# Kernel optimization log

Hardware: AMD Instinct MI355X
Metric: run time of the kernel (lower is better)

Reference implementation:

```python
import jax, jax.numpy as jnp
import numpy as np

N = 100000      # nodes
E = 1600000     # edges
F_IN = 64       # num_features
H = 64          # nhid
G = 512         # num graphs in batch
C = 2           # num_classes
BN_EPS = 1e-5


def setup_inputs() -> dict:
    key = jax.random.key(0)
    ks = jax.random.split(key, 8)
    x = jax.random.normal(ks[0], (N, F_IN), jnp.float32)
    edge_index = jax.random.randint(ks[1], (2, E), 0, N, dtype=jnp.int64)
    batch = jnp.sort(jax.random.randint(ks[2], (N,), 0, G, dtype=jnp.int64))
    s = lambda k, shp, fan: (jax.random.normal(k, shp, jnp.float32) / np.sqrt(fan)).astype(jnp.float32)
    W1 = s(ks[3], (F_IN, H), F_IN); b1 = jnp.zeros((H,), jnp.float32)
    W2 = s(ks[4], (H, H), H);       b2 = jnp.zeros((H,), jnp.float32)
    Wg = s(ks[5], (H, 1), H);       bg = jnp.zeros((1,), jnp.float32)
    bn_gamma = jnp.ones((H,), jnp.float32); bn_beta = jnp.zeros((H,), jnp.float32)
    bn_mean = jnp.zeros((H,), jnp.float32); bn_var = jnp.ones((H,), jnp.float32)
    W_lin = s(ks[6], (H, C), H);    b_lin = jnp.zeros((C,), jnp.float32)
    return dict(x=x, edge_index=edge_index, batch=batch,
                W1=W1, b1=b1, W2=W2, b2=b2, Wg=Wg, bg=bg,
                bn_gamma=bn_gamma, bn_beta=bn_beta, bn_mean=bn_mean, bn_var=bn_var,
                W_lin=W_lin, b_lin=b_lin)


def reference(x, edge_index, batch, W1, b1, W2, b2, Wg, bg,
              bn_gamma, bn_beta, bn_mean, bn_var, W_lin, b_lin):
    src, dst = edge_index[0], edge_index[1]
    # GINConv (eps=0): h_i = MLP(x_i + sum_{j->i} x_j)
    agg = jax.ops.segment_sum(x[src], dst, num_segments=N)       # [N, F_IN]
    h = x + agg
    h = jnp.maximum(h @ W1 + b1, 0.0) @ W2 + b2                  # [N, H]
    h = jnp.maximum(h, 0.0)                                      # outer ReLU
    # Attentional aggregation: segment softmax of gate, weighted segment-sum
    gate = (h @ Wg + bg)[:, 0]                                   # [N]
    gmax = jax.ops.segment_max(gate, batch, num_segments=G)      # [G]
    ex = jnp.exp(gate - gmax[batch])                             # [N]
    denom = jax.ops.segment_sum(ex, batch, num_segments=G)       # [G]
    alpha = ex / denom[batch]                                    # [N]
    pooled = jax.ops.segment_sum(alpha[:, None] * h, batch, num_segments=G)  # [G, H]
    # BatchNorm1d in eval mode (running stats); dropout is identity in eval
    norm = (pooled - bn_mean) / jnp.sqrt(bn_var + BN_EPS) * bn_gamma + bn_beta
    logits = norm @ W_lin + b_lin                                # [G, C]
    return jax.nn.log_softmax(logits, axis=-1)
```

## Files before the change

### kernel.cpp

```cpp
#include <hip/hip_runtime.h>
#include <math.h>
#include <float.h>

#define BN_EPS 1e-5f
#define PBLK   8192
#define NBUCKP 832
#define ACAP   4096
#define STCAP  3072

typedef short s16x8 __attribute__((ext_vector_type(8)));
typedef float f32x4 __attribute__((ext_vector_type(4)));

__device__ __forceinline__ unsigned short f2bf(float f) {
    unsigned u = __float_as_uint(f);
    u += 0x7FFFu + ((u >> 16) & 1u);
    return (unsigned short)(u >> 16);
}
__device__ __forceinline__ float bf2f(unsigned short b) {
    return __uint_as_float(((unsigned)b) << 16);
}

__global__ __launch_bounds__(256) void prep_partition(
    const float* __restrict__ x, unsigned short* __restrict__ xb,
    const float* __restrict__ W1, const float* __restrict__ W2,
    unsigned short* __restrict__ w1t, unsigned short* __restrict__ w2t,
    const int* __restrict__ src, const int* __restrict__ dst,
    int* __restrict__ bcur0, int* __restrict__ packed2,
    int N, int E)
{
    __shared__ int hist[NBUCKP], lstart[NBUCKP], goff[NBUCKP], cur[NBUCKP];
    __shared__ int sorted[PBLK];
    __shared__ unsigned short sbkt[PBLK];

    int tid = threadIdx.x;
    int lane = tid & 63;
    int blk = blockIdx.x;

    int n4 = N * 16;
    for (int i = blk * 256 + tid; i < n4; i += gridDim.x * 256) {
        float4 f = *(const float4*)(x + (size_t)i * 4);
        ushort4 o;
        o.x = f2bf(f.x); o.y = f2bf(f.y); o.z = f2bf(f.z); o.w = f2bf(f.w);
        *(ushort4*)(xb + (size_t)i * 4) = o;
    }
    if (blk == 0)
        for (int idx = tid; idx < 4096; idx += 256)
            w1t[idx] = f2bf(W1[(idx & 63) * 64 + (idx >> 6)]);
    if (blk == 1)
        for (int idx = tid; idx < 4096; idx += 256)
            w2t[idx] = f2bf(W2[(idx & 63) * 64 + (idx >> 6)]);

    int e0 = blk * PBLK;
    int cnt = E - e0; if (cnt > PBLK) cnt = PBLK; if (cnt < 0) cnt = 0;

    for (int i = tid; i < NBUCKP; i += 256) hist[i] = 0;
    __syncthreads();
    for (int i = tid; i < cnt; i += 256)
        atomicAdd(&hist[dst[e0 + i] >> 7], 1);
    __syncthreads();
    if (tid < 64) {
        int carry = 0;
        #pragma unroll
        for (int c = 0; c < NBUCKP / 64; ++c) {
            int idx = c * 64 + lane;
            int v = hist[idx];
            int xv = v;
            #pragma unroll
            for (int d = 1; d < 64; d <<= 1) {
                int t = __shfl_up(xv, d); if (lane >= d) xv += t;
            }
            lstart[idx] = xv - v + carry;
            carry += __shfl(xv, 63);
        }
    }
    __syncthreads();
    for (int i = tid; i < NBUCKP; i += 256) {
        cur[i] = lstart[i];
        if (hist[i] > 0) goff[i] = atomicAdd(&bcur0[i], hist[i]);
    }
    __syncthreads();
    for (int i = tid; i < cnt; i += 256) {
        int d = dst[e0 + i];
        int s = src[e0 + i];
        int b = d >> 7;
        int p = atomicAdd(&cur[b], 1);
        sorted[p] = ((d & 127) << 17) | s;
        sbkt[p] = (unsigned short)b;
    }
    __syncthreads();
    for (int i = tid; i < cnt; i += 256) {
        int b = sbkt[i];
        packed2[(size_t)b * ACAP + goff[b] + (i - lstart[b])] = sorted[i];
    }
}

__global__ __launch_bounds__(512) void bucket_fused(
    const unsigned short* __restrict__ xb,
    const int* __restrict__ packed2, const int* __restrict__ bcur0,
    const unsigned short* __restrict__ w1t, const unsigned short* __restrict__ w2t,
    const float* __restrict__ b1, const float* __restrict__ b2,
    const float* __restrict__ Wg, const float* __restrict__ bg,
    unsigned short* __restrict__ h_out, float* __restrict__ gate_out, int N)
{
    __shared__ int hist[128], excl[129], cur[128];
    __shared__ int stage[STCAP];
    __shared__ unsigned short vt[128][72];

    int tid = threadIdx.x;
    int lane = tid & 63;
    int wave = tid >> 6;
    int b = blockIdx.x;
    int node0 = b * 128;
    int ecnt = bcur0[b];
    const int* arena = packed2 + (size_t)b * ACAP;

    if (tid < 128) hist[tid] = 0;
    __syncthreads();
    for (int i = tid; i < ecnt; i += 512)
        atomicAdd(&hist[arena[i] >> 17], 1);
    __syncthreads();
    if (tid < 64) {
        int carry = 0;
        #pragma unroll
        for (int c = 0; c < 2; ++c) {
            int idx = c * 64 + lane;
            int v = hist[idx];
            int xv = v;
            #pragma unroll
            for (int d = 1; d < 64; d <<= 1) {
                int t = __shfl_up(xv, d); if (lane >= d) xv += t;
            }
            excl[idx] = xv - v + carry;
            carry += __shfl(xv, 63);
        }
        if (lane == 0) excl[128] = carry;
    }
    __syncthreads();
    if (tid < 128) cur[tid] = excl[tid];
    __syncthreads();
    for (int i = tid; i < ecnt; i += 512) {
        int v = arena[i];
        int p = atomicAdd(&cur[v >> 17], 1);
        if (p < STCAP) stage[p] = v & 0x1FFFF;
    }
    __syncthreads();

    int rowbase = wave * 16;
    for (int m = 0; m < 16; ++m) {
        int ln = rowbase + m;
        int node = node0 + ln;
        if (node < N) {
            int beg = excl[ln];     if (beg > STCAP) beg = STCAP;
            int end = excl[ln + 1]; if (end > STCAP) end = STCAP;

            float v0 = bf2f(xb[(size_t)node * 64 + lane]);
            float v1 = 0.f, v2 = 0.f, v3 = 0.f, v4 = 0.f, v5 = 0.f, v6 = 0.f, v7 = 0.f;

            for (int base = beg; base < end; base += 64) {
                int ei = (base + lane < end) ? stage[base + lane] : 0;
                int cnt = end - base; if (cnt > 64) cnt = 64;
                int j = 0;
                for (; j + 8 <= cnt; j += 8) {
                    int s0 = __builtin_amdgcn_readlane(ei, j + 0);
                    int s1 = __builtin_amdgcn_readlane(ei, j + 1);
                    int s2 = __builtin_amdgcn_readlane(ei, j + 2);
                    int s3 = __builtin_amdgcn_readlane(ei, j + 3);
                    int s4 = __builtin_amdgcn_readlane(ei, j + 4);
                    int s5 = __builtin_amdgcn_readlane(ei, j + 5);
                    int s6 = __builtin_amdgcn_readlane(ei, j + 6);
                    int s7 = __builtin_amdgcn_readlane(ei, j + 7);
                    unsigned short t0 = xb[(size_t)s0 * 64 + lane];
                    unsigned short t1 = xb[(size_t)s1 * 64 + lane];
                    unsigned short t2 = xb[(size_t)s2 * 64 + lane];
                    unsigned short t3 = xb[(size_t)s3 * 64 + lane];
                    unsigned short t4 = xb[(size_t)s4 * 64 + lane];
                    unsigned short t5 = xb[(size_t)s5 * 64 + lane];
                    unsigned short t6 = xb[(size_t)s6 * 64 + lane];
                    unsigned short t7 = xb[(size_t)s7 * 64 + lane];
                    v0 += bf2f(t0); v1 += bf2f(t1); v2 += bf2f(t2); v3 += bf2f(t3);
                    v4 += bf2f(t4); v5 += bf2f(t5); v6 += bf2f(t6); v7 += bf2f(t7);
                }
                for (; j < cnt; ++j) {
                    int s = __builtin_amdgcn_readlane(ei, j);
                    v1 += bf2f(xb[(size_t)s * 64 + lane]);
                }
            }
            float v = ((v0 + v1) + (v2 + v3)) + ((v4 + v5) + (v6 + v7));
            vt[ln][lane] = f2bf(v);
        } else {
            vt[ln][lane] = 0;
        }
    }

    {
        int quad = lane >> 4;
        int col  = lane & 15;

        s16x8 a0 = *(const s16x8*)&vt[rowbase + col][quad * 8];
        s16x8 a1 = *(const s16x8*)&vt[rowbase + col][32 + quad * 8];

        float b1v[4], b2v[4], wgv[4];
        #pragma unroll
        for (int nt = 0; nt < 4; ++nt) {
            b1v[nt] = b1[nt * 16 + col];
            b2v[nt] = b2[nt * 16 + col];
            wgv[nt] = Wg[nt * 16 + col];
        }
        float bgv = bg[0];

        f32x4 acc1[4];
        #pragma unroll
        for (int nt = 0; nt < 4; ++nt) {
            int off = (nt * 16 + col) * 64 + quad * 8;
            s16x8 w0 = *(const s16x8*)(w1t + off);
            s16x8 w1 = *(const s16x8*)(w1t + off + 32);
            f32x4 c = {0.f, 0.f, 0.f, 0.f};
            c = __builtin_amdgcn_mfma_f32_16x16x32_bf16(a0, w0, c, 0, 0, 0);
            c = __builtin_amdgcn_mfma_f32_16x16x32_bf16(a1, w1, c, 0, 0, 0);
            acc1[nt] = c;
        }
        #pragma unroll
        for (int nt = 0; nt < 4; ++nt)
            #pragma unroll
            for (int r = 0; r < 4; ++r) {
                float hv = fmaxf(acc1[nt][r] + b1v[nt], 0.f);
                vt[rowbase + quad * 4 + r][nt * 16 + col] = f2bf(hv);
            }

        s16x8 g0 = *(const s16x8*)&vt[rowbase + col][quad * 8];
        s16x8 g1 = *(const s16x8*)&vt[rowbase + col][32 + quad * 8];

        f32x4 acc2[4];
        #pragma unroll
        for (int nt = 0; nt < 4; ++nt) {
            int off = (nt * 16 + col) * 64 + quad * 8;
            s16x8 w0 = *(const s16x8*)(w2t + off);
            s16x8 w1 = *(const s16x8*)(w2t + off + 32);
            f32x4 c = {0.f, 0.f, 0.f, 0.f};
            c = __builtin_amdgcn_mfma_f32_16x16x32_bf16(g0, w0, c, 0, 0, 0);
            c = __builtin_amdgcn_mfma_f32_16x16x32_bf16(g1, w1, c, 0, 0, 0);
            acc2[nt] = c;
        }

        int nbase = node0 + rowbase;
        float gp[4] = {0.f, 0.f, 0.f, 0.f};
        #pragma unroll
        for (int nt = 0; nt < 4; ++nt)
            #pragma unroll
            for (int r = 0; r < 4; ++r) {
                float hv = fmaxf(acc2[nt][r] + b2v[nt], 0.f);
                int node = nbase + quad * 4 + r;
                if (node < N)
                    h_out[(size_t)node * 64 + nt * 16 + col] = f2bf(hv);
                gp[r] = fmaf(hv, wgv[nt], gp[r]);
            }
        #pragma unroll
        for (int r = 0; r < 4; ++r) {
            float t = gp[r];
            t += __shfl_xor(t, 1);
            t += __shfl_xor(t, 2);
            t += __shfl_xor(t, 4);
            t += __shfl_xor(t, 8);
            int node = nbase + quad * 4 + r;
            if (col == 0 && node < N) gate_out[node] = t + bgv;
        }
    }
}

__global__ __launch_bounds__(256) void pool_final(
    const unsigned short* __restrict__ h, const float* __restrict__ gate,
    const int* __restrict__ batch,
    const float* __restrict__ gamma_, const float* __restrict__ beta_,
    const float* __restrict__ mean_, const float* __restrict__ var_,
    const float* __restrict__ Wl, const float* __restrict__ bl,
    float* __restrict__ out, int N)
{
    int g = blockIdx.x;
    int tid = threadIdx.x;

    int lo = 0, hi = N;
    while (lo < hi) { int mid = (lo + hi) >> 1; if (batch[mid] < g) lo = mid + 1; else hi = mid; }
    int start = lo;
    hi = N;
    while (lo < hi) { int mid = (lo + hi) >> 1; if (batch[mid] < g + 1) lo = mid + 1; else hi = mid; }
    int end = lo;

    __shared__ float red[4];
    __shared__ float pool_s[4 * 64];

    int lane = tid & 63;
    int wave = tid >> 6;

    float m = -FLT_MAX;
    for (int i = start + tid; i < end; i += 256) m = fmaxf(m, gate[i]);
    #pragma unroll
    for (int off = 32; off; off >>= 1) m = fmaxf(m, __shfl_xor(m, off));
    if (lane == 0) red[wave] = m;
    __syncthreads();
    m = fmaxf(fmaxf(red[0], red[1]), fmaxf(red[2], red[3]));
    __syncthreads();

    float s = 0.f;
    for (int i = start + tid; i < end; i += 256) s += expf(gate[i] - m);
    #pragma unroll
    for (int off = 32; off; off >>= 1) s += __shfl_xor(s, off);
    if (lane == 0) red[wave] = s;
    __syncthreads();
    s = red[0] + red[1] + red[2] + red[3];

    float a0 = 0.f, a1 = 0.f, a2 = 0.f, a3 = 0.f;
    int i = start + wave;
    for (; i + 12 < end; i += 16) {
        float e0 = expf(gate[i]      - m);
        float e1 = expf(gate[i + 4]  - m);
        float e2 = expf(gate[i + 8]  - m);
        float e3 = expf(gate[i + 12] - m);
        float t0 = bf2f(h[(size_t)(i)      * 64 + lane]);
        float t1 = bf2f(h[(size_t)(i + 4)  * 64 + lane]);
        float t2 = bf2f(h[(size_t)(i + 8)  * 64 + lane]);
        float t3 = bf2f(h[(size_t)(i + 12) * 64 + lane]);
        a0 = fmaf(e0, t0, a0);
        a1 = fmaf(e1, t1, a1);
        a2 = fmaf(e2, t2, a2);
        a3 = fmaf(e3, t3, a3);
    }
    for (; i < end; i += 4) {
        float e = expf(gate[i] - m);
        a0 = fmaf(e, bf2f(h[(size_t)i * 64 + lane]), a0);
    }
    pool_s[wave * 64 + lane] = (a0 + a1) + (a2 + a3);
    __syncthreads();

    if (wave == 0) {
        float p = pool_s[lane] + pool_s[64 + lane] + pool_s[128 + lane] + pool_s[192 + lane];
        p = (end > start) ? (p / s) : 0.f;
        float nrm = (p - mean_[lane]) / sqrtf(var_[lane] + BN_EPS) * gamma_[lane] + beta_[lane];
        float l0 = nrm * Wl[lane * 2 + 0];
        float l1 = nrm * Wl[lane * 2 + 1];
        #pragma unroll
        for (int off = 32; off; off >>= 1) {
            l0 += __shfl_xor(l0, off);
            l1 += __shfl_xor(l1, off);
        }
        if (lane == 0) {
            l0 += bl[0];
            l1 += bl[1];
            float mx = fmaxf(l0, l1);
            float lse = mx + logf(expf(l0 - mx) + expf(l1 - mx));
            out[g * 2 + 0] = l0 - lse;
            out[g * 2 + 1] = l1 - lse;
        }
    }
}

extern "C" void kernel_launch(void* const* d_in, const int* in_sizes, int n_in,
                              void* d_out, int out_size, void* d_ws, size_t ws_size,
                              hipStream_t stream)
{
    const float* x     = (const float*)d_in[0];
    const int*   eidx  = (const int*)d_in[1];
    const int*   batch = (const int*)d_in[2];
    const float* W1    = (const float*)d_in[3];
    const float* b1    = (const float*)d_in[4];
    const float* W2    = (const float*)d_in[5];
    const float* b2    = (const float*)d_in[6];
    const float* Wg    = (const float*)d_in[7];
    const float* bg    = (const float*)d_in[8];
    const float* bng   = (const float*)d_in[9];
    const float* bnb   = (const float*)d_in[10];
    const float* bnm   = (const float*)d_in[11];
    const float* bnv   = (const float*)d_in[12];
    const float* Wl    = (const float*)d_in[13];
    const float* bl    = (const float*)d_in[14];
    float* out = (float*)d_out;

    int N = in_sizes[0] / 64;
    int E = in_sizes[1] / 2;
    int G = out_size / 2;
    int NP = ((N + 63) / 64) * 64;
    int NBUCK = (N + 127) / 128;
    int EB = (E + PBLK - 1) / PBLK;

    char* w = (char*)d_ws;
    int* packed2 = (int*)w;                     w += (size_t)NBUCK * ACAP * 4;
    unsigned short* hxb  = (unsigned short*)w;  w += (size_t)NP * 64 * 2;
    float* gate  = (float*)w;                   w += ((size_t)N * 4 + 255) / 256 * 256;
    int* bcur0   = (int*)w;                     w += NBUCKP * 4;
    unsigned short* w1t = (unsigned short*)w;   w += 4096 * 2;
    unsigned short* w2t = (unsigned short*)w;

    const int* src = eidx;
    const int* dst = eidx + E;

    hipMemsetAsync(bcur0, 0, NBUCKP * sizeof(int), stream);

    prep_partition<<<EB, 256, 0, stream>>>(x, hxb, W1, W2, w1t, w2t,
                                           src, dst, bcur0, packed2, N, E);

    unsigned short* hbuf = w2t + 4096;

    bucket_fused  <<<NBUCK, 512, 0, stream>>>(hxb, packed2, bcur0, w1t, w2t,
                                              b1, b2, Wg, bg, hbuf, gate, N);

    pool_final    <<<G, 256, 0, stream>>>(hbuf, gate, batch, bng, bnb, bnm, bnv,
                                          Wl, bl, out, N);
}
```

Measured before the change: 215.1 us.

## Halve node bucket size and unroll neighbor gather sixteen-wide with clamped lanes

Buckets now cover 64 nodes instead of 128, which doubles the number of fused-kernel blocks and halves block size to 256 threads, with arena and staging capacities shrunk to match. The arena is copied once into shared memory (reusing the vt buffer) so the second scatter pass avoids a repeated global read, and the prefix scan collapses to one wave pass. The neighbor gather loop issues 16 independent loads per iteration, clamping indices and masking the tail, to expose more memory-level parallelism. This adds more partition buckets and wasted loads on partial groups, and the smaller capacities raise the risk of overflowing per-bucket edge space.

```diff
diff --git a/kernel.cpp b/kernel.cpp
--- a/kernel.cpp
+++ b/kernel.cpp
@@ -4,9 +4,9 @@
 
 #define BN_EPS 1e-5f
 #define PBLK   8192
-#define NBUCKP 832
-#define ACAP   4096
-#define STCAP  3072
+#define NBUCKP 1664
+#define ACAP   2048
+#define STCAP  1536
 
 typedef short s16x8 __attribute__((ext_vector_type(8)));
 typedef float f32x4 __attribute__((ext_vector_type(4)));
@@ -56,7 +56,7 @@
     for (int i = tid; i < NBUCKP; i += 256) hist[i] = 0;
     __syncthreads();
     for (int i = tid; i < cnt; i += 256)
-        atomicAdd(&hist[dst[e0 + i] >> 7], 1);
+        atomicAdd(&hist[dst[e0 + i] >> 6], 1);
     __syncthreads();
     if (tid < 64) {
         int carry = 0;
@@ -82,9 +82,9 @@
     for (int i = tid; i < cnt; i += 256) {
         int d = dst[e0 + i];
         int s = src[e0 + i];
-        int b = d >> 7;
+        int b = d >> 6;
         int p = atomicAdd(&cur[b], 1);
-        sorted[p] = ((d & 127) << 17) | s;
+        sorted[p] = ((d & 63) << 17) | s;
         sbkt[p] = (unsigned short)b;
     }
     __syncthreads();
@@ -94,7 +94,7 @@
     }
 }
 
-__global__ __launch_bounds__(512) void bucket_fused(
+__global__ __launch_bounds__(256) void bucket_fused(
     const unsigned short* __restrict__ xb,
     const int* __restrict__ packed2, const int* __restrict__ bcur0,
     const unsigned short* __restrict__ w1t, const unsigned short* __restrict__ w2t,
@@ -102,44 +102,42 @@
     const float* __restrict__ Wg, const float* __restrict__ bg,
     unsigned short* __restrict__ h_out, float* __restrict__ gate_out, int N)
 {
-    __shared__ int hist[128], excl[129], cur[128];
+    __shared__ int hist[64], excl[65], cur[64];
     __shared__ int stage[STCAP];
-    __shared__ unsigned short vt[128][72];
+    __shared__ unsigned short vt[64][72];
 
     int tid = threadIdx.x;
     int lane = tid & 63;
     int wave = tid >> 6;
     int b = blockIdx.x;
-    int node0 = b * 128;
+    int node0 = b * 64;
     int ecnt = bcur0[b];
+    if (ecnt > ACAP) ecnt = ACAP;
     const int* arena = packed2 + (size_t)b * ACAP;
-
-    if (tid < 128) hist[tid] = 0;
-    __syncthreads();
-    for (int i = tid; i < ecnt; i += 512)
-        atomicAdd(&hist[arena[i] >> 17], 1);
+    int* raw = (int*)vt;
+
+    if (tid < 64) hist[tid] = 0;
+    __syncthreads();
+    for (int i = tid; i < ecnt; i += 256) {
+        int v = arena[i];
+        raw[i] = v;
+        atomicAdd(&hist[v >> 17], 1);
+    }
     __syncthreads();
     if (tid < 64) {
-        int carry = 0;
-        #pragma unroll
-        for (int c = 0; c < 2; ++c) {
-            int idx = c * 64 + lane;
-            int v = hist[idx];
-            int xv = v;
-            #pragma unroll
-            for (int d = 1; d < 64; d <<= 1) {
-                int t = __shfl_up(xv, d); if (lane >= d) xv += t;
-            }
-            excl[idx] = xv - v + carry;
-            carry += __shfl(xv, 63);
-        }
-        if (lane == 0) excl[128] = carry;
-    }
-    __syncthreads();
-    if (tid < 128) cur[tid] = excl[tid];
-    __syncthreads();
-    for (int i = tid; i < ecnt; i += 512) {
-        int v = arena[i];
+        int v = hist[lane];
+        int xv = v;
+        #pragma unroll
+        for (int d = 1; d < 64; d <<= 1) {
+            int t = __shfl_up(xv, d); if (lane >= d) xv += t;
+        }
+        excl[lane] = xv - v;
+        if (lane == 63) excl[64] = xv;
+        cur[lane] = xv - v;
+    }
+    __syncthreads();
+    for (int i = tid; i < ecnt; i += 256) {
+        int v = raw[i];
         int p = atomicAdd(&cur[v >> 17], 1);
         if (p < STCAP) stage[p] = v & 0x1FFFF;
     }
@@ -149,47 +147,40 @@
     for (int m = 0; m < 16; ++m) {
         int ln = rowbase + m;
         int node = node0 + ln;
-        if (node < N) {
-            int beg = excl[ln];     if (beg > STCAP) beg = STCAP;
-            int end = excl[ln + 1]; if (end > STCAP) end = STCAP;
-
-            float v0 = bf2f(xb[(size_t)node * 64 + lane]);
-            float v1 = 0.f, v2 = 0.f, v3 = 0.f, v4 = 0.f, v5 = 0.f, v6 = 0.f, v7 = 0.f;
-
-            for (int base = beg; base < end; base += 64) {
-                int ei = (base + lane < end) ? stage[base + lane] : 0;
-                int cnt = end - base; if (cnt > 64) cnt = 64;
-                int j = 0;
-                for (; j + 8 <= cnt; j += 8) {
-                    int s0 = __builtin_amdgcn_readlane(ei, j + 0);
-                    int s1 = __builtin_amdgcn_readlane(ei, j + 1);
-                    int s2 = __builtin_amdgcn_readlane(ei, j + 2);
-                    int s3 = __builtin_amdgcn_readlane(ei, j + 3);
-                    int s4 = __builtin_amdgcn_readlane(ei, j + 4);
-                    int s5 = __builtin_amdgcn_readlane(ei, j + 5);
-                    int s6 = __builtin_amdgcn_readlane(ei, j + 6);
-                    int s7 = __builtin_amdgcn_readlane(ei, j + 7);
-                    unsigned short t0 = xb[(size_t)s0 * 64 + lane];
-                    unsigned short t1 = xb[(size_t)s1 * 64 + lane];
-                    unsigned short t2 = xb[(size_t)s2 * 64 + lane];
-                    unsigned short t3 = xb[(size_t)s3 * 64 + lane];
-                    unsigned short t4 = xb[(size_t)s4 * 64 + lane];
-                    unsigned short t5 = xb[(size_t)s5 * 64 + lane];
-                    unsigned short t6 = xb[(size_t)s6 * 64 + lane];
-                    unsigned short t7 = xb[(size_t)s7 * 64 + lane];
-                    v0 += bf2f(t0); v1 += bf2f(t1); v2 += bf2f(t2); v3 += bf2f(t3);
-                    v4 += bf2f(t4); v5 += bf2f(t5); v6 += bf2f(t6); v7 += bf2f(t7);
+        if (node >= N) { vt[ln][lane] = 0; continue; }
+        int beg = excl[ln];     if (beg > STCAP) beg = STCAP;
+        int end = excl[ln + 1]; if (end > STCAP) end = STCAP;
+
+        float acc[16];
+        acc[0] = bf2f(xb[(size_t)node * 64 + lane]);
+        #pragma unroll
+        for (int q = 1; q < 16; ++q) acc[q] = 0.f;
+
+        for (int base = beg; base < end; base += 64) {
+            int ei = (base + lane < end) ? stage[base + lane] : 0;
+            int cnt = end - base; if (cnt > 64) cnt = 64;
+            int lim = cnt - 1;
+            for (int j = 0; j < cnt; j += 16) {
+                int s[16];
+                unsigned short t[16];
+                #pragma unroll
+                for (int q = 0; q < 16; ++q) {
+                    int idx = j + q; if (idx > lim) idx = lim;
+                    s[q] = __builtin_amdgcn_readlane(ei, idx);
                 }
-                for (; j < cnt; ++j) {
-                    int s = __builtin_amdgcn_readlane(ei, j);
-                    v1 += bf2f(xb[(size_t)s * 64 + lane]);
-                }
+                #pragma unroll
+                for (int q = 0; q < 16; ++q)
+                    t[q] = xb[(size_t)s[q] * 64 + lane];
+                #pragma unroll
+                for (int q = 0; q < 16; ++q)
+                    acc[q] += (j + q < cnt) ? bf2f(t[q]) : 0.f;
             }
-            float v = ((v0 + v1) + (v2 + v3)) + ((v4 + v5) + (v6 + v7));
-            vt[ln][lane] = f2bf(v);
-        } else {
-            vt[ln][lane] = 0;
-        }
+        }
+        float v = ((acc[0] + acc[1]) + (acc[2] + acc[3]))
+                + ((acc[4] + acc[5]) + (acc[6] + acc[7]))
+                + ((acc[8] + acc[9]) + (acc[10] + acc[11]))
+                + ((acc[12] + acc[13]) + (acc[14] + acc[15]));
+        vt[ln][lane] = f2bf(v);
     }
 
     {
@@ -378,7 +369,7 @@
     int E = in_sizes[1] / 2;
     int G = out_size / 2;
     int NP = ((N + 63) / 64) * 64;
-    int NBUCK = (N + 127) / 128;
+    int NBUCK = (N + 63) / 64;
     int EB = (E + PBLK - 1) / PBLK;
 
     char* w = (char*)d_ws;
@@ -387,7 +378,8 @@
     float* gate  = (float*)w;                   w += ((size_t)N * 4 + 255) / 256 * 256;
     int* bcur0   = (int*)w;                     w += NBUCKP * 4;
     unsigned short* w1t = (unsigned short*)w;   w += 4096 * 2;
-    unsigned short* w2t = (unsigned short*)w;
+    unsigned short* w2t = (unsigned short*)w;   w += 4096 * 2;
+    unsigned short* hbuf = (unsigned short*)w;
 
     const int* src = eidx;
     const int* dst = eidx + E;
@@ -397,9 +389,7 @@
     prep_partition<<<EB, 256, 0, stream>>>(x, hxb, W1, W2, w1t, w2t,
                                            src, dst, bcur0, packed2, N, E);
 
-    unsigned short* hbuf = w2t + 4096;
-
-    bucket_fused  <<<NBUCK, 512, 0, stream>>>(hxb, packed2, bcur0, w1t, w2t,
+    bucket_fused  <<<NBUCK, 256, 0, stream>>>(hxb, packed2, bcur0, w1t, w2t,
                                               b1, b2, Wg, bg, hbuf, gate, N);
 
     pool_final    <<<G, 256, 0, stream>>>(hbuf, gate, batch, bng, bnb, bnm, bnv,
```

New measurement: 226.9 us. 5.5% more time.
